# Performance work log

Hardware: AMD Instinct MI355X
Metric: run time of the kernel (lower is better)

Reference implementation:

```python
import jax, jax.numpy as jnp
import numpy as np

COMMITMENT_COST = 0.25
NUM_EMBEDDINGS = 8192
EMBEDDING_DIM = 256


def setup_inputs() -> dict:
    key = jax.random.key(0)
    kx, ke = jax.random.split(key)
    x = jax.random.normal(kx, (16, 1024, EMBEDDING_DIM), dtype=jnp.float32)
    # nn.Embedding weight initialized uniform(-1/K, 1/K)
    embedding = jax.random.uniform(
        ke, (NUM_EMBEDDINGS, EMBEDDING_DIM), dtype=jnp.float32,
        minval=-1.0 / NUM_EMBEDDINGS, maxval=1.0 / NUM_EMBEDDINGS)
    return {"x": x, "embedding": embedding}


def reference(x, embedding):
    x_shape = x.shape
    D = embedding.shape[1]
    K = embedding.shape[0]
    flat_x = x.reshape(-1, D)                      # [N, D]
    N = flat_x.shape[0]

    distances = (jnp.sum(flat_x ** 2, axis=1, keepdims=True)
                 + jnp.sum(embedding ** 2, axis=1)
                 - 2.0 * jnp.matmul(flat_x, embedding.T))
    encoding_indices = jnp.argmin(distances, axis=1)  # [N]

    # one-hot @ embedding == gather
    quantized = embedding[encoding_indices].reshape(x_shape)

    sg = jax.lax.stop_gradient
    e_latent_loss = jnp.mean((sg(quantized) - x) ** 2)
    q_latent_loss = jnp.mean((quantized - sg(x)) ** 2)
    loss = q_latent_loss + COMMITMENT_COST * e_latent_loss

    # straight-through estimator
    quantized_st = x + sg(quantized - x)

    # perplexity from mean one-hot usage
    counts = jnp.zeros((K,), dtype=jnp.float32).at[encoding_indices].add(1.0)
    avg_probs = counts / N
    perplexity = jnp.exp(-jnp.sum(avg_probs * jnp.log(avg_probs + 1e-10)))

    return quantized_st.reshape(x_shape), loss, perplexity
```

## Files before the change

### kernel.cpp

```cpp
#include <hip/hip_runtime.h>


#define VQ_N 16384
#define VQ_D 256
#define VQ_K 8192

typedef __attribute__((ext_vector_type(4))) int i32x4;

#define SX 22.0f
#define SEF 1040384.0f
#define ENSCALE 11444224.0

__device__ inline int q8(float f, float scale) {
  return __float2int_rn(fminf(fmaxf(f * scale, -127.f), 127.f));
}

__global__ __launch_bounds__(256) void vq_pack(
    const float* __restrict__ E, signed char* __restrict__ Ebs,
    int* __restrict__ en_int, double* __restrict__ loss_sum,
    int* __restrict__ hist, unsigned int* __restrict__ ticket) {
  const int gid = blockIdx.x * 256 + threadIdx.x;
  if (gid < VQ_K) hist[gid] = 0;
  if (gid == 0) { *loss_sum = 0.0; *ticket = 0u; }
  const int code = gid >> 4;
  const int chunk = gid & 15;
  const float* src = E + (size_t)code * VQ_D + chunk * 16;
  double s = 0.0;
  unsigned int w[4];
#pragma unroll
  for (int v = 0; v < 4; ++v) {
    const float4 f = *(const float4*)(src + v * 4);
    s += (double)f.x * f.x + (double)f.y * f.y + (double)f.z * f.z +
         (double)f.w * f.w;
    const int q0 = q8(f.x, SEF), q1 = q8(f.y, SEF);
    const int q2 = q8(f.z, SEF), q3 = q8(f.w, SEF);
    w[v] = (unsigned)(q0 & 255) | ((unsigned)(q1 & 255) << 8) |
           ((unsigned)(q2 & 255) << 16) | ((unsigned)(q3 & 255) << 24);
  }
  const size_t off =
      ((size_t)(code >> 4) * 16 + chunk) * 256 + (size_t)(code & 15) * 16;
  *(uint4*)(Ebs + off) = make_uint4(w[0], w[1], w[2], w[3]);
#pragma unroll
  for (int m = 1; m <= 8; m <<= 1) s += __shfl_xor(s, m, 64);
  if (chunk == 0) en_int[code] = (int)__double2int_rn(s * ENSCALE);
}

__global__ __launch_bounds__(256, 1) void vq_main(
    const float* __restrict__ X, const signed char* __restrict__ Ebs,
    const int* __restrict__ en_int, const float* __restrict__ Ef,
    float* __restrict__ outq, double* __restrict__ loss_sum,
    int* __restrict__ hist, unsigned int* __restrict__ ticket,
    float* __restrict__ out) {
  __shared__ int red_s[4][64];
  __shared__ int red_i[4][64];
  __shared__ int kfin[64];
  __shared__ double wsum[4];
  __shared__ double part[256];
  __shared__ int sdone;

  const int tid = threadIdx.x;
  const int wave = tid >> 6;
  const int lane = tid & 63;
  const int quad = lane >> 4;
  const int c15 = lane & 15;
  const int r0 = blockIdx.x * 64;

  i32x4 af[4][4];
#pragma unroll
  for (int t = 0; t < 4; ++t) {
    const float* xr = X + (size_t)(r0 + t * 16 + c15) * VQ_D + quad * 16;
#pragma unroll
    for (int m = 0; m < 4; ++m) {
      const float* p = xr + m * 64;
      i32x4 pk;
#pragma unroll
      for (int v = 0; v < 4; ++v) {
        const float4 f = *(const float4*)(p + v * 4);
        const int q0 = q8(f.x, SX), q1 = q8(f.y, SX);
        const int q2 = q8(f.z, SX), q3 = q8(f.w, SX);
        pk[v] = (q0 & 255) | ((q1 & 255) << 8) | ((q2 & 255) << 16) |
                ((q3 & 255) << 24);
      }
      af[t][m] = pk;
    }
  }

  int best_s[4][4];
  int best_i[4][4];
#pragma unroll
  for (int t = 0; t < 4; ++t)
#pragma unroll
    for (int r = 0; r < 4; ++r) { best_s[t][r] = 0x7fffffff; best_i[t][r] = 0; }

  const signed char* bp =
      Ebs + (size_t)wave * 4096 + (size_t)quad * 256 + (size_t)c15 * 16;
  const int* enp = en_int + wave * 16 + c15;
  int lidx = 0;
  int ccode = wave * 16 + c15;

#define LOADB(buf, en)                                                       \
  {                                                                          \
    const signed char* p_ = bp + (size_t)lidx * 16384;                       \
    _Pragma("unroll") for (int m = 0; m < 4; ++m)                            \
        buf[m] = *(const i32x4*)(p_ + m * 1024);                             \
    en = enp[lidx * 64];                                                     \
    ++lidx;                                                                  \
  }

#define COMPUTE(buf, en)                                                     \
  {                                                                          \
    i32x4 a0 = {0, 0, 0, 0}, a1 = {0, 0, 0, 0};                              \
    i32x4 a2 = {0, 0, 0, 0}, a3 = {0, 0, 0, 0};                              \
    _Pragma("unroll") for (int m = 0; m < 4; ++m) {                          \
      a0 = __builtin_amdgcn_mfma_i32_16x16x64_i8(af[0][m], buf[m], a0, 0, 0, 0); \
      a1 = __builtin_amdgcn_mfma_i32_16x16x64_i8(af[1][m], buf[m], a1, 0, 0, 0); \
      a2 = __builtin_amdgcn_mfma_i32_16x16x64_i8(af[2][m], buf[m], a2, 0, 0, 0); \
      a3 = __builtin_amdgcn_mfma_i32_16x16x64_i8(af[3][m], buf[m], a3, 0, 0, 0); \
    }                                                                        \
    _Pragma("unroll") for (int r = 0; r < 4; ++r) {                          \
      int s;                                                                 \
      s = en - a0[r];                                                        \
      if (s < best_s[0][r]) { best_s[0][r] = s; best_i[0][r] = ccode; }      \
      s = en - a1[r];                                                        \
      if (s < best_s[1][r]) { best_s[1][r] = s; best_i[1][r] = ccode; }      \
      s = en - a2[r];                                                        \
      if (s < best_s[2][r]) { best_s[2][r] = s; best_i[2][r] = ccode; }      \
      s = en - a3[r];                                                        \
      if (s < best_s[3][r]) { best_s[3][r] = s; best_i[3][r] = ccode; }      \
    }                                                                        \
    ccode += 64;                                                             \
  }

  i32x4 bb0[4], bb1[4], bb2[4], bb3[4];
  int en0, en1, en2, en3;
  LOADB(bb0, en0); LOADB(bb1, en1); LOADB(bb2, en2); LOADB(bb3, en3);
#pragma unroll 1
  for (int i = 0; i < 124; i += 4) {
    COMPUTE(bb0, en0); LOADB(bb0, en0);
    COMPUTE(bb1, en1); LOADB(bb1, en1);
    COMPUTE(bb2, en2); LOADB(bb2, en2);
    COMPUTE(bb3, en3); LOADB(bb3, en3);
  }
  COMPUTE(bb0, en0); COMPUTE(bb1, en1); COMPUTE(bb2, en2); COMPUTE(bb3, en3);
#undef LOADB
#undef COMPUTE

#pragma unroll
  for (int t = 0; t < 4; ++t)
#pragma unroll
    for (int r = 0; r < 4; ++r) {
      int s = best_s[t][r];
      int i = best_i[t][r];
#pragma unroll
      for (int m = 1; m <= 8; m <<= 1) {
        const int os = __shfl_xor(s, m, 64);
        const int oi = __shfl_xor(i, m, 64);
        if (os < s || (os == s && oi < i)) { s = os; i = oi; }
      }
      if (c15 == 0) {
        red_s[wave][t * 16 + quad * 4 + r] = s;
        red_i[wave][t * 16 + quad * 4 + r] = i;
      }
    }
  __syncthreads();

  if (tid < 64) {
    int bs = red_s[0][tid];
    int bi = red_i[0][tid];
#pragma unroll
    for (int w = 1; w < 4; ++w) {
      const int s = red_s[w][tid];
      const int i = red_i[w][tid];
      if (s < bs || (s == bs && i < bi)) { bs = s; bi = i; }
    }
    kfin[tid] = bi;
    __hip_atomic_fetch_add(&hist[bi], 1, __ATOMIC_RELAXED,
                           __HIP_MEMORY_SCOPE_AGENT);
  }
  __syncthreads();

  double lacc = 0.0;
#pragma unroll
  for (int j = 0; j < 16; ++j) {
    const int rl = wave * 16 + j;
    const int k = kfin[rl];
    const float4 q = *(const float4*)(Ef + (size_t)k * VQ_D + lane * 4);
    const float4 x =
        *(const float4*)(X + (size_t)(r0 + rl) * VQ_D + lane * 4);
    *(float4*)(outq + (size_t)(r0 + rl) * VQ_D + lane * 4) = q;
    const double dx = (double)q.x - x.x, dy = (double)q.y - x.y;
    const double dz = (double)q.z - x.z, dw = (double)q.w - x.w;
    lacc += dx * dx + dy * dy + dz * dz + dw * dw;
  }
#pragma unroll
  for (int off = 32; off > 0; off >>= 1) lacc += __shfl_down(lacc, off, 64);
  if (lane == 0) wsum[wave] = lacc;
  __syncthreads();
  if (tid == 0) {
    atomicAdd(loss_sum, wsum[0] + wsum[1] + wsum[2] + wsum[3]);
    __threadfence();
    const unsigned int old = __hip_atomic_fetch_add(
        ticket, 1u, __ATOMIC_ACQ_REL, __HIP_MEMORY_SCOPE_AGENT);
    sdone = (old == 255u) ? 1 : 0;
  }
  __syncthreads();

  if (sdone) {
    double s = 0.0;
    for (int k = tid; k < VQ_K; k += 256) {
      const int c = __hip_atomic_load(&hist[k], __ATOMIC_RELAXED,
                                      __HIP_MEMORY_SCOPE_AGENT);
      if (c > 0) {
        const double pr = (double)c * (1.0 / (double)VQ_N);
        s += pr * log(pr + 1e-10);
      }
    }
    part[tid] = s;
    __syncthreads();
    for (int off = 128; off > 0; off >>= 1) {
      if (tid < off) part[tid] += part[tid + off];
      __syncthreads();
    }
    if (tid == 0) {
      const double ls = __hip_atomic_load(loss_sum, __ATOMIC_RELAXED,
                                          __HIP_MEMORY_SCOPE_AGENT);
      out[(size_t)VQ_N * VQ_D] =
          (float)(1.25 * ls / ((double)VQ_N * (double)VQ_D));
      out[(size_t)VQ_N * VQ_D + 1] = (float)exp(-part[0]);
    }
  }
}

extern "C" void kernel_launch(void* const* d_in, const int* in_sizes, int n_in,
                              void* d_out, int out_size, void* d_ws,
                              size_t ws_size, hipStream_t stream) {
  const float* X = (const float*)d_in[0];
  const float* E = (const float*)d_in[1];
  float* out = (float*)d_out;

  char* ws = (char*)d_ws;
  signed char* Ebs = (signed char*)ws;
  int* en_int = (int*)(ws + 2097152);
  double* loss_sum = (double*)(ws + 2129920);
  int* hist = (int*)(ws + 2129984);
  unsigned int* ticket = (unsigned int*)(ws + 2162752);

  vq_pack<<<512, 256, 0, stream>>>(E, Ebs, en_int, loss_sum, hist, ticket);
  vq_main<<<256, 256, 0, stream>>>(X, Ebs, en_int, E, out, loss_sum, hist,
                                   ticket, out);
}
```

Baseline: 160.7 us.

## Split codebook across 16 waves per block and pack score with index

The main kernel now launches 1024 threads per block, so 16 waves each scan a quarter as many codebook slices for the same 64 rows. The X tile is quantized once cooperatively into LDS and each wave reads its int8 A fragments from there. The argmin key is packed as (score<<8 | slice index), so a single min replaces compare-and-select, and the prefetch depth drops from 4 to 2 buffers. This trades more per-block parallelism and fewer registers for a wider cross-wave reduction and shifted scores that could lose precision or overflow if scores exceed 24 bits.

Measured after the change: 169.6 us. 5.6% more time.

```diff
diff --git a/kernel.cpp b/kernel.cpp
--- a/kernel.cpp
+++ b/kernel.cpp
@@ -45,17 +45,18 @@
   if (chunk == 0) en_int[code] = (int)__double2int_rn(s * ENSCALE);
 }
 
-__global__ __launch_bounds__(256, 1) void vq_main(
+__global__ __launch_bounds__(1024) void vq_main(
     const float* __restrict__ X, const signed char* __restrict__ Ebs,
     const int* __restrict__ en_int, const float* __restrict__ Ef,
     float* __restrict__ outq, double* __restrict__ loss_sum,
     int* __restrict__ hist, unsigned int* __restrict__ ticket,
     float* __restrict__ out) {
-  __shared__ int red_s[4][64];
-  __shared__ int red_i[4][64];
+  __shared__ __align__(16) signed char alds[64 * 272];
+  __shared__ int red_s[16][64];
+  __shared__ int red_i[16][64];
   __shared__ int kfin[64];
-  __shared__ double wsum[4];
-  __shared__ double part[256];
+  __shared__ double wsum[16];
+  __shared__ double part[1024];
   __shared__ int sdone;
 
   const int tid = threadIdx.x;
@@ -65,83 +66,73 @@
   const int c15 = lane & 15;
   const int r0 = blockIdx.x * 64;
 
+  {
+    const int qrow = wave * 4 + quad;
+    const float* xs = X + (size_t)(r0 + qrow) * VQ_D + c15 * 16;
+    i32x4 pk;
+#pragma unroll
+    for (int v = 0; v < 4; ++v) {
+      const float4 f = *(const float4*)(xs + v * 4);
+      const int q0 = q8(f.x, SX), q1 = q8(f.y, SX);
+      const int q2 = q8(f.z, SX), q3 = q8(f.w, SX);
+      pk[v] = (q0 & 255) | ((q1 & 255) << 8) | ((q2 & 255) << 16) |
+              ((q3 & 255) << 24);
+    }
+    *(i32x4*)(alds + qrow * 272 + c15 * 16) = pk;
+  }
+  __syncthreads();
+
   i32x4 af[4][4];
 #pragma unroll
-  for (int t = 0; t < 4; ++t) {
-    const float* xr = X + (size_t)(r0 + t * 16 + c15) * VQ_D + quad * 16;
-#pragma unroll
-    for (int m = 0; m < 4; ++m) {
-      const float* p = xr + m * 64;
-      i32x4 pk;
-#pragma unroll
-      for (int v = 0; v < 4; ++v) {
-        const float4 f = *(const float4*)(p + v * 4);
-        const int q0 = q8(f.x, SX), q1 = q8(f.y, SX);
-        const int q2 = q8(f.z, SX), q3 = q8(f.w, SX);
-        pk[v] = (q0 & 255) | ((q1 & 255) << 8) | ((q2 & 255) << 16) |
-                ((q3 & 255) << 24);
-      }
-      af[t][m] = pk;
-    }
-  }
-
-  int best_s[4][4];
-  int best_i[4][4];
-#pragma unroll
   for (int t = 0; t < 4; ++t)
 #pragma unroll
-    for (int r = 0; r < 4; ++r) { best_s[t][r] = 0x7fffffff; best_i[t][r] = 0; }
+    for (int m = 0; m < 4; ++m)
+      af[t][m] =
+          *(const i32x4*)(alds + (t * 16 + c15) * 272 + m * 64 + quad * 16);
+
+  int best[4][4];
+#pragma unroll
+  for (int t = 0; t < 4; ++t)
+#pragma unroll
+    for (int r = 0; r < 4; ++r) best[t][r] = 0x7fffffff;
 
   const signed char* bp =
       Ebs + (size_t)wave * 4096 + (size_t)quad * 256 + (size_t)c15 * 16;
   const int* enp = en_int + wave * 16 + c15;
   int lidx = 0;
-  int ccode = wave * 16 + c15;
-
-#define LOADB(buf, en)                                                       \
+
+#define LOADB(buf, enk)                                                      \
   {                                                                          \
-    const signed char* p_ = bp + (size_t)lidx * 16384;                       \
+    const signed char* p_ = bp + (size_t)lidx * 65536;                       \
     _Pragma("unroll") for (int m = 0; m < 4; ++m)                            \
         buf[m] = *(const i32x4*)(p_ + m * 1024);                             \
-    en = enp[lidx * 64];                                                     \
+    enk = (int)((unsigned)enp[lidx * 256] << 8) + lidx;                      \
     ++lidx;                                                                  \
   }
 
-#define COMPUTE(buf, en)                                                     \
+#define COMPUTE(buf, enk)                                                    \
   {                                                                          \
-    i32x4 a0 = {0, 0, 0, 0}, a1 = {0, 0, 0, 0};                              \
-    i32x4 a2 = {0, 0, 0, 0}, a3 = {0, 0, 0, 0};                              \
-    _Pragma("unroll") for (int m = 0; m < 4; ++m) {                          \
-      a0 = __builtin_amdgcn_mfma_i32_16x16x64_i8(af[0][m], buf[m], a0, 0, 0, 0); \
-      a1 = __builtin_amdgcn_mfma_i32_16x16x64_i8(af[1][m], buf[m], a1, 0, 0, 0); \
-      a2 = __builtin_amdgcn_mfma_i32_16x16x64_i8(af[2][m], buf[m], a2, 0, 0, 0); \
-      a3 = __builtin_amdgcn_mfma_i32_16x16x64_i8(af[3][m], buf[m], a3, 0, 0, 0); \
+    _Pragma("unroll") for (int t = 0; t < 4; ++t) {                          \
+      i32x4 acc = {0, 0, 0, 0};                                              \
+      _Pragma("unroll") for (int m = 0; m < 4; ++m)                          \
+          acc = __builtin_amdgcn_mfma_i32_16x16x64_i8(af[t][m], buf[m], acc, \
+                                                      0, 0, 0);              \
+      _Pragma("unroll") for (int r = 0; r < 4; ++r) {                        \
+        const int cand = (enk) - (int)((unsigned)acc[r] << 8);               \
+        best[t][r] = min(best[t][r], cand);                                  \
+      }                                                                      \
     }                                                                        \
-    _Pragma("unroll") for (int r = 0; r < 4; ++r) {                          \
-      int s;                                                                 \
-      s = en - a0[r];                                                        \
-      if (s < best_s[0][r]) { best_s[0][r] = s; best_i[0][r] = ccode; }      \
-      s = en - a1[r];                                                        \
-      if (s < best_s[1][r]) { best_s[1][r] = s; best_i[1][r] = ccode; }      \
-      s = en - a2[r];                                                        \
-      if (s < best_s[2][r]) { best_s[2][r] = s; best_i[2][r] = ccode; }      \
-      s = en - a3[r];                                                        \
-      if (s < best_s[3][r]) { best_s[3][r] = s; best_i[3][r] = ccode; }      \
-    }                                                                        \
-    ccode += 64;                                                             \
-  }
-
-  i32x4 bb0[4], bb1[4], bb2[4], bb3[4];
-  int en0, en1, en2, en3;
-  LOADB(bb0, en0); LOADB(bb1, en1); LOADB(bb2, en2); LOADB(bb3, en3);
+  }
+
+  i32x4 bb0[4], bb1[4];
+  int ek0, ek1;
+  LOADB(bb0, ek0); LOADB(bb1, ek1);
 #pragma unroll 1
-  for (int i = 0; i < 124; i += 4) {
-    COMPUTE(bb0, en0); LOADB(bb0, en0);
-    COMPUTE(bb1, en1); LOADB(bb1, en1);
-    COMPUTE(bb2, en2); LOADB(bb2, en2);
-    COMPUTE(bb3, en3); LOADB(bb3, en3);
-  }
-  COMPUTE(bb0, en0); COMPUTE(bb1, en1); COMPUTE(bb2, en2); COMPUTE(bb3, en3);
+  for (int i = 0; i < 30; i += 2) {
+    COMPUTE(bb0, ek0); LOADB(bb0, ek0);
+    COMPUTE(bb1, ek1); LOADB(bb1, ek1);
+  }
+  COMPUTE(bb0, ek0); COMPUTE(bb1, ek1);
 #undef LOADB
 #undef COMPUTE
 
@@ -149,8 +140,9 @@
   for (int t = 0; t < 4; ++t)
 #pragma unroll
     for (int r = 0; r < 4; ++r) {
-      int s = best_s[t][r];
-      int i = best_i[t][r];
+      const int key = best[t][r];
+      int s = key >> 8;
+      int i = ((key & 255) << 8) + wave * 16 + c15;
 #pragma unroll
       for (int m = 1; m <= 8; m <<= 1) {
         const int os = __shfl_xor(s, m, 64);
@@ -168,7 +160,7 @@
     int bs = red_s[0][tid];
     int bi = red_i[0][tid];
 #pragma unroll
-    for (int w = 1; w < 4; ++w) {
+    for (int w = 1; w < 16; ++w) {
       const int s = red_s[w][tid];
       const int i = red_i[w][tid];
       if (s < bs || (s == bs && i < bi)) { bs = s; bi = i; }
@@ -181,8 +173,8 @@
 
   double lacc = 0.0;
 #pragma unroll
-  for (int j = 0; j < 16; ++j) {
-    const int rl = wave * 16 + j;
+  for (int j = 0; j < 4; ++j) {
+    const int rl = wave * 4 + j;
     const int k = kfin[rl];
     const float4 q = *(const float4*)(Ef + (size_t)k * VQ_D + lane * 4);
     const float4 x =
@@ -197,7 +189,10 @@
   if (lane == 0) wsum[wave] = lacc;
   __syncthreads();
   if (tid == 0) {
-    atomicAdd(loss_sum, wsum[0] + wsum[1] + wsum[2] + wsum[3]);
+    double ws = 0.0;
+#pragma unroll
+    for (int w = 0; w < 16; ++w) ws += wsum[w];
+    atomicAdd(loss_sum, ws);
     __threadfence();
     const unsigned int old = __hip_atomic_fetch_add(
         ticket, 1u, __ATOMIC_ACQ_REL, __HIP_MEMORY_SCOPE_AGENT);
@@ -207,7 +202,7 @@
 
   if (sdone) {
     double s = 0.0;
-    for (int k = tid; k < VQ_K; k += 256) {
+    for (int k = tid; k < VQ_K; k += 1024) {
       const int c = __hip_atomic_load(&hist[k], __ATOMIC_RELAXED,
                                       __HIP_MEMORY_SCOPE_AGENT);
       if (c > 0) {
@@ -217,7 +212,7 @@
     }
     part[tid] = s;
     __syncthreads();
-    for (int off = 128; off > 0; off >>= 1) {
+    for (int off = 512; off > 0; off >>= 1) {
       if (tid < off) part[tid] += part[tid + off];
       __syncthreads();
     }
@@ -246,6 +241,6 @@
   unsigned int* ticket = (unsigned int*)(ws + 2162752);
 
   vq_pack<<<512, 256, 0, stream>>>(E, Ebs, en_int, loss_sum, hist, ticket);
-  vq_main<<<256, 256, 0, stream>>>(X, Ebs, en_int, E, out, loss_sum, hist,
-                                   ticket, out);
-}
+  vq_main<<<256, 1024, 0, stream>>>(X, Ebs, en_int, E, out, loss_sum, hist,
+                                    ticket, out);
+}
```

## Split codebook across four slices per row group with ticketed cross-block argmin merge

Applied to the files above, without the earlier changes.

The codebook search is split into four slices of 2048 codes, and the grid grows from 256 to 1024 blocks so more CUs run at once. Each block writes its partial argmin candidates to workspace. The last block to arrive for a row group, detected through an atomic ticket, merges the four candidates and runs the gather, loss and histogram epilogue. This adds global round-trips, fences and redundant quantisation of X per slice in exchange for better occupancy across the 256 CUs.

Result: slower. 208.6 us (+29.8%).

```diff
diff --git a/kernel.cpp b/kernel.cpp
--- a/kernel.cpp
+++ b/kernel.cpp
@@ -18,9 +18,11 @@
 __global__ __launch_bounds__(256) void vq_pack(
     const float* __restrict__ E, signed char* __restrict__ Ebs,
     int* __restrict__ en_int, double* __restrict__ loss_sum,
-    int* __restrict__ hist, unsigned int* __restrict__ ticket) {
+    int* __restrict__ hist, unsigned int* __restrict__ ticket,
+    unsigned int* __restrict__ rowticket) {
   const int gid = blockIdx.x * 256 + threadIdx.x;
   if (gid < VQ_K) hist[gid] = 0;
+  if (gid < 256) rowticket[gid] = 0u;
   if (gid == 0) { *loss_sum = 0.0; *ticket = 0u; }
   const int code = gid >> 4;
   const int chunk = gid & 15;
@@ -50,12 +52,14 @@
     const int* __restrict__ en_int, const float* __restrict__ Ef,
     float* __restrict__ outq, double* __restrict__ loss_sum,
     int* __restrict__ hist, unsigned int* __restrict__ ticket,
-    float* __restrict__ out) {
+    unsigned int* __restrict__ rowticket, int* __restrict__ cand_s,
+    int* __restrict__ cand_i, float* __restrict__ out) {
   __shared__ int red_s[4][64];
   __shared__ int red_i[4][64];
   __shared__ int kfin[64];
   __shared__ double wsum[4];
   __shared__ double part[256];
+  __shared__ int smerge;
   __shared__ int sdone;
 
   const int tid = threadIdx.x;
@@ -63,7 +67,9 @@
   const int lane = tid & 63;
   const int quad = lane >> 4;
   const int c15 = lane & 15;
-  const int r0 = blockIdx.x * 64;
+  const int rg = blockIdx.x & 255;
+  const int slice = blockIdx.x >> 8;
+  const int r0 = rg * 64;
 
   i32x4 af[4][4];
 #pragma unroll
@@ -92,11 +98,12 @@
 #pragma unroll
     for (int r = 0; r < 4; ++r) { best_s[t][r] = 0x7fffffff; best_i[t][r] = 0; }
 
-  const signed char* bp =
-      Ebs + (size_t)wave * 4096 + (size_t)quad * 256 + (size_t)c15 * 16;
-  const int* enp = en_int + wave * 16 + c15;
+  const signed char* bp = Ebs + (size_t)slice * 524288 +
+                          (size_t)wave * 4096 + (size_t)quad * 256 +
+                          (size_t)c15 * 16;
+  const int* enp = en_int + slice * 2048 + wave * 16 + c15;
   int lidx = 0;
-  int ccode = wave * 16 + c15;
+  int ccode = slice * 2048 + wave * 16 + c15;
 
 #define LOADB(buf, en)                                                       \
   {                                                                          \
@@ -135,7 +142,7 @@
   int en0, en1, en2, en3;
   LOADB(bb0, en0); LOADB(bb1, en1); LOADB(bb2, en2); LOADB(bb3, en3);
 #pragma unroll 1
-  for (int i = 0; i < 124; i += 4) {
+  for (int i = 0; i < 28; i += 4) {
     COMPUTE(bb0, en0); LOADB(bb0, en0);
     COMPUTE(bb1, en1); LOADB(bb1, en1);
     COMPUTE(bb2, en2); LOADB(bb2, en2);
@@ -171,6 +178,28 @@
     for (int w = 1; w < 4; ++w) {
       const int s = red_s[w][tid];
       const int i = red_i[w][tid];
+      if (s < bs || (s == bs && i < bi)) { bs = s; bi = i; }
+    }
+    cand_s[rg * 256 + slice * 64 + tid] = bs;
+    cand_i[rg * 256 + slice * 64 + tid] = bi;
+  }
+  __syncthreads();
+  if (tid == 0) {
+    __threadfence();
+    const unsigned int old = __hip_atomic_fetch_add(
+        &rowticket[rg], 1u, __ATOMIC_ACQ_REL, __HIP_MEMORY_SCOPE_AGENT);
+    smerge = (old == 3u) ? 1 : 0;
+  }
+  __syncthreads();
+  if (!smerge) return;
+
+  if (tid < 64) {
+    int bs = cand_s[rg * 256 + tid];
+    int bi = cand_i[rg * 256 + tid];
+#pragma unroll
+    for (int s4 = 1; s4 < 4; ++s4) {
+      const int s = cand_s[rg * 256 + s4 * 64 + tid];
+      const int i = cand_i[rg * 256 + s4 * 64 + tid];
       if (s < bs || (s == bs && i < bi)) { bs = s; bi = i; }
     }
     kfin[tid] = bi;
@@ -244,8 +273,12 @@
   double* loss_sum = (double*)(ws + 2129920);
   int* hist = (int*)(ws + 2129984);
   unsigned int* ticket = (unsigned int*)(ws + 2162752);
-
-  vq_pack<<<512, 256, 0, stream>>>(E, Ebs, en_int, loss_sum, hist, ticket);
-  vq_main<<<256, 256, 0, stream>>>(X, Ebs, en_int, E, out, loss_sum, hist,
-                                   ticket, out);
-}
+  unsigned int* rowticket = (unsigned int*)(ws + 2162816);
+  int* cand_s = (int*)(ws + 2163840);
+  int* cand_i = (int*)(ws + 2425984);
+
+  vq_pack<<<512, 256, 0, stream>>>(E, Ebs, en_int, loss_sum, hist, ticket,
+                                   rowticket);
+  vq_main<<<1024, 256, 0, stream>>>(X, Ebs, en_int, E, out, loss_sum, hist,
+                                    ticket, rowticket, cand_s, cand_i, out);
+}
```

## Split codebook across blocks with LDS-resident slices and separate epilogue kernel

Applied to the files above, without the earlier changes.

X is now pre-quantized to int8 in the pack kernel, and the main kernel is reorganized so each block holds a 512-code slice of the int8 codebook (128 KB) in LDS and scans 1024 rows against it. Per-slice argmin candidates are written to global memory and reduced by a new epilogue kernel that also does the gather, loss and histogram. The argmin update packs score and local group index into one int key, which replaces the compare-and-select with a plain min. This removes repeated streaming of the whole codebook from global memory by every block. It costs an extra kernel launch, an extra X pass and a candidate buffer round trip, and the shift by 8 may lose score range.

Result: slower. 177.9 us (+10.7%).

```diff
diff --git a/kernel.cpp b/kernel.cpp
--- a/kernel.cpp
+++ b/kernel.cpp
@@ -16,163 +16,181 @@
 }
 
 __global__ __launch_bounds__(256) void vq_pack(
-    const float* __restrict__ E, signed char* __restrict__ Ebs,
+    const float* __restrict__ E, const float* __restrict__ X,
+    signed char* __restrict__ Ebs, signed char* __restrict__ Xq,
     int* __restrict__ en_int, double* __restrict__ loss_sum,
     int* __restrict__ hist, unsigned int* __restrict__ ticket) {
   const int gid = blockIdx.x * 256 + threadIdx.x;
   if (gid < VQ_K) hist[gid] = 0;
   if (gid == 0) { *loss_sum = 0.0; *ticket = 0u; }
-  const int code = gid >> 4;
-  const int chunk = gid & 15;
-  const float* src = E + (size_t)code * VQ_D + chunk * 16;
-  double s = 0.0;
-  unsigned int w[4];
-#pragma unroll
-  for (int v = 0; v < 4; ++v) {
-    const float4 f = *(const float4*)(src + v * 4);
-    s += (double)f.x * f.x + (double)f.y * f.y + (double)f.z * f.z +
-         (double)f.w * f.w;
-    const int q0 = q8(f.x, SEF), q1 = q8(f.y, SEF);
-    const int q2 = q8(f.z, SEF), q3 = q8(f.w, SEF);
-    w[v] = (unsigned)(q0 & 255) | ((unsigned)(q1 & 255) << 8) |
-           ((unsigned)(q2 & 255) << 16) | ((unsigned)(q3 & 255) << 24);
-  }
-  const size_t off =
-      ((size_t)(code >> 4) * 16 + chunk) * 256 + (size_t)(code & 15) * 16;
-  *(uint4*)(Ebs + off) = make_uint4(w[0], w[1], w[2], w[3]);
-#pragma unroll
-  for (int m = 1; m <= 8; m <<= 1) s += __shfl_xor(s, m, 64);
-  if (chunk == 0) en_int[code] = (int)__double2int_rn(s * ENSCALE);
+  if (gid < 131072) {
+    const int code = gid >> 4;
+    const int chunk = gid & 15;
+    const float* src = E + (size_t)code * VQ_D + chunk * 16;
+    double s = 0.0;
+    unsigned int w[4];
+#pragma unroll
+    for (int v = 0; v < 4; ++v) {
+      const float4 f = *(const float4*)(src + v * 4);
+      s += (double)f.x * f.x + (double)f.y * f.y + (double)f.z * f.z +
+           (double)f.w * f.w;
+      const int q0 = q8(f.x, SEF), q1 = q8(f.y, SEF);
+      const int q2 = q8(f.z, SEF), q3 = q8(f.w, SEF);
+      w[v] = (unsigned)(q0 & 255) | ((unsigned)(q1 & 255) << 8) |
+             ((unsigned)(q2 & 255) << 16) | ((unsigned)(q3 & 255) << 24);
+    }
+    const size_t off =
+        ((size_t)(code >> 4) * 16 + chunk) * 256 + (size_t)(code & 15) * 16;
+    *(uint4*)(Ebs + off) = make_uint4(w[0], w[1], w[2], w[3]);
+#pragma unroll
+    for (int m = 1; m <= 8; m <<= 1) s += __shfl_xor(s, m, 64);
+    if (chunk == 0) en_int[code] = (int)__double2int_rn(s * ENSCALE);
+  } else {
+    const int xid = gid - 131072;
+    const int row = xid >> 4;
+    const int chunk = xid & 15;
+    const float* src = X + (size_t)row * VQ_D + chunk * 16;
+    unsigned int w[4];
+#pragma unroll
+    for (int v = 0; v < 4; ++v) {
+      const float4 f = *(const float4*)(src + v * 4);
+      const int q0 = q8(f.x, SX), q1 = q8(f.y, SX);
+      const int q2 = q8(f.z, SX), q3 = q8(f.w, SX);
+      w[v] = (unsigned)(q0 & 255) | ((unsigned)(q1 & 255) << 8) |
+             ((unsigned)(q2 & 255) << 16) | ((unsigned)(q3 & 255) << 24);
+    }
+    const size_t off =
+        ((size_t)(row >> 4) * 16 + chunk) * 256 + (size_t)(row & 15) * 16;
+    *(uint4*)(Xq + off) = make_uint4(w[0], w[1], w[2], w[3]);
+  }
 }
 
 __global__ __launch_bounds__(256, 1) void vq_main(
-    const float* __restrict__ X, const signed char* __restrict__ Ebs,
-    const int* __restrict__ en_int, const float* __restrict__ Ef,
-    float* __restrict__ outq, double* __restrict__ loss_sum,
-    int* __restrict__ hist, unsigned int* __restrict__ ticket,
-    float* __restrict__ out) {
-  __shared__ int red_s[4][64];
-  __shared__ int red_i[4][64];
-  __shared__ int kfin[64];
-  __shared__ double wsum[4];
-  __shared__ double part[256];
-  __shared__ int sdone;
+    const signed char* __restrict__ Ebs, const signed char* __restrict__ Xq,
+    const int* __restrict__ en_int, long long* __restrict__ cand) {
+  __shared__ __align__(16) signed char Blds[131072];
+  __shared__ int ens[512];
 
   const int tid = threadIdx.x;
   const int wave = tid >> 6;
   const int lane = tid & 63;
   const int quad = lane >> 4;
   const int c15 = lane & 15;
-  const int r0 = blockIdx.x * 64;
-
-  i32x4 af[4][4];
-#pragma unroll
-  for (int t = 0; t < 4; ++t) {
-    const float* xr = X + (size_t)(r0 + t * 16 + c15) * VQ_D + quad * 16;
-#pragma unroll
-    for (int m = 0; m < 4; ++m) {
-      const float* p = xr + m * 64;
-      i32x4 pk;
-#pragma unroll
-      for (int v = 0; v < 4; ++v) {
-        const float4 f = *(const float4*)(p + v * 4);
-        const int q0 = q8(f.x, SX), q1 = q8(f.y, SX);
-        const int q2 = q8(f.z, SX), q3 = q8(f.w, SX);
-        pk[v] = (q0 & 255) | ((q1 & 255) << 8) | ((q2 & 255) << 16) |
-                ((q3 & 255) << 24);
-      }
-      af[t][m] = pk;
-    }
-  }
-
-  int best_s[4][4];
-  int best_i[4][4];
-#pragma unroll
-  for (int t = 0; t < 4; ++t)
-#pragma unroll
-    for (int r = 0; r < 4; ++r) { best_s[t][r] = 0x7fffffff; best_i[t][r] = 0; }
-
-  const signed char* bp =
-      Ebs + (size_t)wave * 4096 + (size_t)quad * 256 + (size_t)c15 * 16;
-  const int* enp = en_int + wave * 16 + c15;
-  int lidx = 0;
-  int ccode = wave * 16 + c15;
-
-#define LOADB(buf, en)                                                       \
+  const int rg = blockIdx.x & 15;
+  const int slice = blockIdx.x >> 4;
+
+  {
+    const signed char* src = Ebs + (size_t)slice * 131072;
+#pragma unroll 4
+    for (int it = 0; it < 32; ++it) {
+      const int off = it * 4096 + tid * 16;
+      *(i32x4*)(Blds + off) = *(const i32x4*)(src + off);
+    }
+    if (tid < 128) {
+      const int4 e4 = *(const int4*)(en_int + slice * 512 + tid * 4);
+      *(int4*)(ens + tid * 4) = e4;
+    }
+  }
+  __syncthreads();
+
+  const int wrow0 = rg * 1024 + wave * 256;
+
+#pragma unroll 1
+  for (int rr = 0; rr < 4; ++rr) {
+    const signed char* ap = Xq + (size_t)(wrow0 + rr * 64) * 256;
+    i32x4 af[4][4];
+#pragma unroll
+    for (int t = 0; t < 4; ++t)
+#pragma unroll
+      for (int m = 0; m < 4; ++m)
+        af[t][m] = *(const i32x4*)(ap + t * 4096 + m * 1024 + lane * 16);
+
+    int best[4][4];
+#pragma unroll
+    for (int t = 0; t < 4; ++t)
+#pragma unroll
+      for (int r = 0; r < 4; ++r) best[t][r] = 0x7fffffff;
+
+    i32x4 bfA[4], bfB[4];
+#pragma unroll
+    for (int m = 0; m < 4; ++m)
+      bfA[m] = *(const i32x4*)(Blds + m * 1024 + lane * 16);
+
+#define GBODY(CUR, NXT, g)                                                   \
   {                                                                          \
-    const signed char* p_ = bp + (size_t)lidx * 16384;                       \
+    const int gn_ = ((g) + 1) & 31;                                          \
     _Pragma("unroll") for (int m = 0; m < 4; ++m)                            \
-        buf[m] = *(const i32x4*)(p_ + m * 1024);                             \
-    en = enp[lidx * 64];                                                     \
-    ++lidx;                                                                  \
-  }
-
-#define COMPUTE(buf, en)                                                     \
-  {                                                                          \
+        NXT[m] = *(const i32x4*)(Blds + gn_ * 4096 + m * 1024 + lane * 16);  \
+    const int enk_ = (ens[(g) * 16 + c15] << 8) | (g);                       \
     i32x4 a0 = {0, 0, 0, 0}, a1 = {0, 0, 0, 0};                              \
     i32x4 a2 = {0, 0, 0, 0}, a3 = {0, 0, 0, 0};                              \
     _Pragma("unroll") for (int m = 0; m < 4; ++m) {                          \
-      a0 = __builtin_amdgcn_mfma_i32_16x16x64_i8(af[0][m], buf[m], a0, 0, 0, 0); \
-      a1 = __builtin_amdgcn_mfma_i32_16x16x64_i8(af[1][m], buf[m], a1, 0, 0, 0); \
-      a2 = __builtin_amdgcn_mfma_i32_16x16x64_i8(af[2][m], buf[m], a2, 0, 0, 0); \
-      a3 = __builtin_amdgcn_mfma_i32_16x16x64_i8(af[3][m], buf[m], a3, 0, 0, 0); \
+      a0 = __builtin_amdgcn_mfma_i32_16x16x64_i8(af[0][m], CUR[m], a0, 0, 0, 0); \
+      a1 = __builtin_amdgcn_mfma_i32_16x16x64_i8(af[1][m], CUR[m], a1, 0, 0, 0); \
+      a2 = __builtin_amdgcn_mfma_i32_16x16x64_i8(af[2][m], CUR[m], a2, 0, 0, 0); \
+      a3 = __builtin_amdgcn_mfma_i32_16x16x64_i8(af[3][m], CUR[m], a3, 0, 0, 0); \
     }                                                                        \
     _Pragma("unroll") for (int r = 0; r < 4; ++r) {                          \
-      int s;                                                                 \
-      s = en - a0[r];                                                        \
-      if (s < best_s[0][r]) { best_s[0][r] = s; best_i[0][r] = ccode; }      \
-      s = en - a1[r];                                                        \
-      if (s < best_s[1][r]) { best_s[1][r] = s; best_i[1][r] = ccode; }      \
-      s = en - a2[r];                                                        \
-      if (s < best_s[2][r]) { best_s[2][r] = s; best_i[2][r] = ccode; }      \
-      s = en - a3[r];                                                        \
-      if (s < best_s[3][r]) { best_s[3][r] = s; best_i[3][r] = ccode; }      \
+      best[0][r] = min(best[0][r], enk_ - (int)((unsigned)a0[r] << 8));      \
+      best[1][r] = min(best[1][r], enk_ - (int)((unsigned)a1[r] << 8));      \
+      best[2][r] = min(best[2][r], enk_ - (int)((unsigned)a2[r] << 8));      \
+      best[3][r] = min(best[3][r], enk_ - (int)((unsigned)a3[r] << 8));      \
     }                                                                        \
-    ccode += 64;                                                             \
-  }
-
-  i32x4 bb0[4], bb1[4], bb2[4], bb3[4];
-  int en0, en1, en2, en3;
-  LOADB(bb0, en0); LOADB(bb1, en1); LOADB(bb2, en2); LOADB(bb3, en3);
+  }
+
 #pragma unroll 1
-  for (int i = 0; i < 124; i += 4) {
-    COMPUTE(bb0, en0); LOADB(bb0, en0);
-    COMPUTE(bb1, en1); LOADB(bb1, en1);
-    COMPUTE(bb2, en2); LOADB(bb2, en2);
-    COMPUTE(bb3, en3); LOADB(bb3, en3);
-  }
-  COMPUTE(bb0, en0); COMPUTE(bb1, en1); COMPUTE(bb2, en2); COMPUTE(bb3, en3);
-#undef LOADB
-#undef COMPUTE
-
-#pragma unroll
-  for (int t = 0; t < 4; ++t)
-#pragma unroll
-    for (int r = 0; r < 4; ++r) {
-      int s = best_s[t][r];
-      int i = best_i[t][r];
-#pragma unroll
-      for (int m = 1; m <= 8; m <<= 1) {
-        const int os = __shfl_xor(s, m, 64);
-        const int oi = __shfl_xor(i, m, 64);
-        if (os < s || (os == s && oi < i)) { s = os; i = oi; }
+    for (int gg = 0; gg < 32; gg += 2) {
+      GBODY(bfA, bfB, gg);
+      GBODY(bfB, bfA, gg + 1);
+    }
+#undef GBODY
+
+#pragma unroll
+    for (int t = 0; t < 4; ++t)
+#pragma unroll
+      for (int r = 0; r < 4; ++r) {
+        const int key = best[t][r];
+        int s = key >> 8;
+        int i = slice * 512 + ((key & 255) << 4) + c15;
+#pragma unroll
+        for (int m = 1; m <= 8; m <<= 1) {
+          const int os = __shfl_xor(s, m, 64);
+          const int oi = __shfl_xor(i, m, 64);
+          if (os < s || (os == s && oi < i)) { s = os; i = oi; }
+        }
+        if (c15 == 0) {
+          const int row = wrow0 + rr * 64 + t * 16 + quad * 4 + r;
+          cand[(size_t)row * 16 + slice] =
+              ((long long)s << 32) | (unsigned int)i;
+        }
       }
-      if (c15 == 0) {
-        red_s[wave][t * 16 + quad * 4 + r] = s;
-        red_i[wave][t * 16 + quad * 4 + r] = i;
-      }
-    }
-  __syncthreads();
+  }
+}
+
+__global__ __launch_bounds__(256) void vq_epi(
+    const float* __restrict__ X, const float* __restrict__ Ef,
+    const long long* __restrict__ cand, float* __restrict__ outq,
+    double* __restrict__ loss_sum, int* __restrict__ hist,
+    unsigned int* __restrict__ ticket, float* __restrict__ out) {
+  __shared__ int kfin[64];
+  __shared__ double wsum[4];
+  __shared__ double part[256];
+  __shared__ int sdone;
+
+  const int tid = threadIdx.x;
+  const int wave = tid >> 6;
+  const int lane = tid & 63;
+  const int r0 = blockIdx.x * 64;
 
   if (tid < 64) {
-    int bs = red_s[0][tid];
-    int bi = red_i[0][tid];
-#pragma unroll
-    for (int w = 1; w < 4; ++w) {
-      const int s = red_s[w][tid];
-      const int i = red_i[w][tid];
-      if (s < bs || (s == bs && i < bi)) { bs = s; bi = i; }
-    }
+    const long long* cp = cand + (size_t)(r0 + tid) * 16;
+    long long b = cp[0];
+#pragma unroll
+    for (int sl = 1; sl < 16; ++sl) {
+      const long long v = cp[sl];
+      b = (v < b) ? v : b;
+    }
+    const int bi = (int)(b & 0xffffffffll);
     kfin[tid] = bi;
     __hip_atomic_fetch_add(&hist[bi], 1, __ATOMIC_RELAXED,
                            __HIP_MEMORY_SCOPE_AGENT);
@@ -240,12 +258,16 @@
 
   char* ws = (char*)d_ws;
   signed char* Ebs = (signed char*)ws;
-  int* en_int = (int*)(ws + 2097152);
-  double* loss_sum = (double*)(ws + 2129920);
-  int* hist = (int*)(ws + 2129984);
-  unsigned int* ticket = (unsigned int*)(ws + 2162752);
-
-  vq_pack<<<512, 256, 0, stream>>>(E, Ebs, en_int, loss_sum, hist, ticket);
-  vq_main<<<256, 256, 0, stream>>>(X, Ebs, en_int, E, out, loss_sum, hist,
-                                   ticket, out);
-}
+  signed char* Xq = (signed char*)(ws + 2097152);
+  int* en_int = (int*)(ws + 6291456);
+  int* hist = (int*)(ws + 6324224);
+  double* loss_sum = (double*)(ws + 6356992);
+  unsigned int* ticket = (unsigned int*)(ws + 6357056);
+  long long* cand = (long long*)(ws + 6357120);
+
+  vq_pack<<<1536, 256, 0, stream>>>(E, X, Ebs, Xq, en_int, loss_sum, hist,
+                                    ticket);
+  vq_main<<<256, 256, 0, stream>>>(Ebs, Xq, en_int, cand);
+  vq_epi<<<256, 256, 0, stream>>>(X, E, cand, out, loss_sum, hist, ticket,
+                                  out);
+}
```
